# Optimization experiments

Measured on AMD Instinct MI355X. Metric: run time of the kernel, lower is better.

## Reference

```python
import jax, jax.numpy as jnp
from jax import lax
import numpy as np

IMG = 28
CENTER = 14  # cv2.circle center (14, 14)
B = 65536
NUM_T = 20


def setup_inputs() -> dict:
    key = jax.random.key(0)
    k1, k2, k3, k4 = jax.random.split(key, 4)
    x = jax.random.normal(k1, (B, 1, IMG, IMG), dtype=jnp.float32)
    t = jax.random.randint(k2, (B,), 0, NUM_T)  # per-sample radius/timestep
    Wk = jax.random.normal(k3, (1, 1, 3, 3), dtype=jnp.float32) * 0.1
    b = jax.random.normal(k4, (1,), dtype=jnp.float32) * 0.1
    return {"x": x, "t": t, "Wk": Wk, "b": b}


def _forward_process(x0, r):
    # Vectorized equivalent of the per-sample cv2.circle masking loop:
    # zero out pixels within radius r of (14, 14); r < 0 -> no masking
    # (covers t-1 when t == 0; cv2 draws nothing for negative radius).
    coords = jnp.arange(IMG)
    dist2 = (coords[:, None] - CENTER) ** 2 + (coords[None, :] - CENTER) ** 2  # [H, W]
    r = r.astype(jnp.int32)
    inside = (dist2[None, None, :, :] <= (r * r)[:, None, None, None]) & (r >= 0)[:, None, None, None]
    return jnp.where(inside, jnp.float32(0), x0)


def _reverse(x, Wk, b):
    # minimal denoiser network: 3x3 conv (SAME) + bias
    y = lax.conv_general_dilated(x, Wk, window_strides=(1, 1), padding='SAME')
    return y + b[None, :, None, None]


def reference(x, t, Wk, b):
    # restore_step_algo2: x - forward_process(x_0, t) + forward_process(x_0, t-1)
    x0 = _reverse(x, Wk, b)
    return x - _forward_process(x0, t) + _forward_process(x0, t - 1)
```

## Files before the change

kernel.cpp:

```cpp
#include <hip/hip_runtime.h>

#define IMG 28
#define NPIX (IMG * IMG)
#define NVEC (NPIX / 4)
#define CENTER 14

__global__ __launch_bounds__(256) void SuperResolution_89876485636254_kernel(
    const float* __restrict__ x,
    const int*   __restrict__ t,
    const float* __restrict__ Wk,
    const float* __restrict__ bias,
    float*       __restrict__ out)
{
    __shared__ float s[4][NPIX];

    const int wave = threadIdx.x >> 6;
    const int lane = threadIdx.x & 63;
    const int img  = blockIdx.x * 4 + wave;

    const float4* __restrict__ xin4 = (const float4*)(x + (size_t)img * NPIX);
    float4*       __restrict__ out4 = (float4*)(out + (size_t)img * NPIX);
    float4*       s4 = (float4*)s[wave];

    float4 vals[4];
    #pragma unroll
    for (int kk = 0; kk < 4; ++kk) {
        int k = lane + kk * 64;
        if (k < NVEC) {
            vals[kk] = xin4[k];
            s4[k]    = vals[kk];
        }
    }

    const int rt  = t[img];
    const int r2  = rt * rt;
    const int r12 = (rt - 1) * (rt - 1);
    float w[9];
    #pragma unroll
    for (int i = 0; i < 9; ++i) w[i] = Wk[i];
    const float bb = bias[0];

    __syncthreads();

    const float* __restrict__ simg = s[wave];

    #pragma unroll
    for (int kk = 0; kk < 4; ++kk) {
        int k = lane + kk * 64;
        if (k < NVEC) {
            float4 v = vals[kk];
            float r[4] = {v.x, v.y, v.z, v.w};
            const int p = 4 * k;
            const int i = p / IMG;
            const int j0 = p - i * IMG;
            const int di = i - CENTER;
            const int di2 = di * di;
            #pragma unroll
            for (int e = 0; e < 4; ++e) {
                const int j  = j0 + e;
                const int dj = j - CENTER;
                const int d2 = di2 + dj * dj;
                const bool in_t  = (d2 <= r2);
                const bool in_t1 = (rt >= 1) && (d2 <= r12);
                if (in_t && !in_t1) {
                    float acc = bb;
                    #pragma unroll
                    for (int a = 0; a < 3; ++a) {
                        const int ii = i + a - 1;
                        if (ii >= 0 && ii < IMG) {
                            #pragma unroll
                            for (int c = 0; c < 3; ++c) {
                                const int jj = j + c - 1;
                                if (jj >= 0 && jj < IMG)
                                    acc += w[a * 3 + c] * simg[ii * IMG + jj];
                            }
                        }
                    }
                    r[e] += acc;
                }
            }
            float4 ov;
            ov.x = r[0]; ov.y = r[1]; ov.z = r[2]; ov.w = r[3];
            out4[k] = ov;
        }
    }
}

extern "C" void kernel_launch(void* const* d_in, const int* in_sizes, int n_in,
                              void* d_out, int out_size, void* d_ws, size_t ws_size,
                              hipStream_t stream) {
    const float* x    = (const float*)d_in[0];
    const int*   t    = (const int*)d_in[1];
    const float* Wk   = (const float*)d_in[2];
    const float* bias = (const float*)d_in[3];
    float*       out  = (float*)d_out;

    const int B = in_sizes[0] / NPIX;
    const int blocks = B / 4;

    SuperResolution_89876485636254_kernel<<<blocks, 256, 0, stream>>>(
        x, t, Wk, bias, out);
}
```

Baseline: 348.3 us.

## Flatten to one float4 per thread, drop LDS staging, read annulus neighbours from global

Each thread now handles one float4 of the flattened batch instead of four per lane within per-wave image tiles. The shared-memory staging and __syncthreads are gone. Threads whose four pixels touch the ring between radius t-1 and t gather their 3x3 neighbours directly from global memory, relying on the cache. Output uses nontemporal stores. This removes the LDS traffic and the barrier and improves occupancy and coalescing, but the few annulus pixels now do redundant global loads and the t/Wk loads are issued per thread.

```diff
diff --git a/kernel.cpp b/kernel.cpp
--- a/kernel.cpp
+++ b/kernel.cpp
@@ -4,6 +4,8 @@
 #define NPIX (IMG * IMG)
 #define NVEC (NPIX / 4)
 #define CENTER 14
+
+typedef float f32x4 __attribute__((ext_vector_type(4)));
 
 __global__ __launch_bounds__(256) void SuperResolution_89876485636254_kernel(
     const float* __restrict__ x,
@@ -12,78 +14,66 @@
     const float* __restrict__ bias,
     float*       __restrict__ out)
 {
-    __shared__ float s[4][NPIX];
+    const int k   = blockIdx.x * 256 + threadIdx.x;
+    const int img = k / NVEC;
+    const int rem = k - img * NVEC;
+    const int p   = rem * 4;
+    const int i   = p / IMG;
+    const int j0  = p - i * IMG;
 
-    const int wave = threadIdx.x >> 6;
-    const int lane = threadIdx.x & 63;
-    const int img  = blockIdx.x * 4 + wave;
-
-    const float4* __restrict__ xin4 = (const float4*)(x + (size_t)img * NPIX);
-    float4*       __restrict__ out4 = (float4*)(out + (size_t)img * NPIX);
-    float4*       s4 = (float4*)s[wave];
-
-    float4 vals[4];
-    #pragma unroll
-    for (int kk = 0; kk < 4; ++kk) {
-        int k = lane + kk * 64;
-        if (k < NVEC) {
-            vals[kk] = xin4[k];
-            s4[k]    = vals[kk];
-        }
-    }
+    const f32x4 v = ((const f32x4*)x)[k];
+    float r[4] = {v.x, v.y, v.z, v.w};
 
     const int rt  = t[img];
     const int r2  = rt * rt;
     const int r12 = (rt - 1) * (rt - 1);
-    float w[9];
+
+    const int di  = i - CENTER;
+    const int di2 = di * di;
+
+    int  d2e[4];
+    bool ann[4];
+    bool any = false;
     #pragma unroll
-    for (int i = 0; i < 9; ++i) w[i] = Wk[i];
-    const float bb = bias[0];
+    for (int e = 0; e < 4; ++e) {
+        const int dj = j0 + e - CENTER;
+        d2e[e] = di2 + dj * dj;
+        ann[e] = (d2e[e] <= r2) && !((rt >= 1) && (d2e[e] <= r12));
+        any = any || ann[e];
+    }
 
-    __syncthreads();
+    if (any) {
+        float w[9];
+        #pragma unroll
+        for (int q = 0; q < 9; ++q) w[q] = Wk[q];
+        const float bb = bias[0];
+        const float* __restrict__ ximg = x + (size_t)img * NPIX;
 
-    const float* __restrict__ simg = s[wave];
-
-    #pragma unroll
-    for (int kk = 0; kk < 4; ++kk) {
-        int k = lane + kk * 64;
-        if (k < NVEC) {
-            float4 v = vals[kk];
-            float r[4] = {v.x, v.y, v.z, v.w};
-            const int p = 4 * k;
-            const int i = p / IMG;
-            const int j0 = p - i * IMG;
-            const int di = i - CENTER;
-            const int di2 = di * di;
-            #pragma unroll
-            for (int e = 0; e < 4; ++e) {
-                const int j  = j0 + e;
-                const int dj = j - CENTER;
-                const int d2 = di2 + dj * dj;
-                const bool in_t  = (d2 <= r2);
-                const bool in_t1 = (rt >= 1) && (d2 <= r12);
-                if (in_t && !in_t1) {
-                    float acc = bb;
-                    #pragma unroll
-                    for (int a = 0; a < 3; ++a) {
-                        const int ii = i + a - 1;
-                        if (ii >= 0 && ii < IMG) {
-                            #pragma unroll
-                            for (int c = 0; c < 3; ++c) {
-                                const int jj = j + c - 1;
-                                if (jj >= 0 && jj < IMG)
-                                    acc += w[a * 3 + c] * simg[ii * IMG + jj];
-                            }
+        #pragma unroll
+        for (int e = 0; e < 4; ++e) {
+            if (ann[e]) {
+                const int j = j0 + e;
+                float acc = bb;
+                #pragma unroll
+                for (int a = 0; a < 3; ++a) {
+                    const int ii = i + a - 1;
+                    if (ii >= 0 && ii < IMG) {
+                        #pragma unroll
+                        for (int c = 0; c < 3; ++c) {
+                            const int jj = j + c - 1;
+                            if (jj >= 0 && jj < IMG)
+                                acc += w[a * 3 + c] * ximg[ii * IMG + jj];
                         }
                     }
-                    r[e] += acc;
                 }
+                r[e] += acc;
             }
-            float4 ov;
-            ov.x = r[0]; ov.y = r[1]; ov.z = r[2]; ov.w = r[3];
-            out4[k] = ov;
         }
     }
+
+    f32x4 ov;
+    ov.x = r[0]; ov.y = r[1]; ov.z = r[2]; ov.w = r[3];
+    __builtin_nontemporal_store(ov, (f32x4*)out + k);
 }
 
 extern "C" void kernel_launch(void* const* d_in, const int* in_sizes, int n_in,
@@ -95,8 +85,9 @@
     const float* bias = (const float*)d_in[3];
     float*       out  = (float*)d_out;
 
-    const int B = in_sizes[0] / NPIX;
-    const int blocks = B / 4;
+    const int B      = in_sizes[0] / NPIX;
+    const int nvec   = B * NVEC;
+    const int blocks = (nvec + 255) / 256;
 
     SuperResolution_89876485636254_kernel<<<blocks, 256, 0, stream>>>(
         x, t, Wk, bias, out);
```

Result: slower. 461.8 us (+32.6%).
